# Performance work log

Hardware: AMD Instinct MI355X
Metric: run time of the kernel (lower is better)

## Reference

```python
import jax, jax.numpy as jnp
import numpy as np

INF_SUB_NUM = -9000000000000000.0
LN_EPS = 1e-5


def _layernorm(x, gamma, beta):
    mu = jnp.mean(x, axis=-1, keepdims=True)
    var = jnp.mean(jnp.square(x - mu), axis=-1, keepdims=True)
    return gamma * (x - mu) * jax.lax.rsqrt(var + LN_EPS) + beta


def setup_inputs() -> dict:
    key = jax.random.key(0)
    kh, ke, kt, kw1, kw2 = jax.random.split(key, 5)
    B, N, E, D = 8, 4096, 2048, 256
    stdv = 1.0 / np.sqrt(D)
    return {
        "hidden": jax.random.normal(kh, (B, N, D), dtype=jnp.float32),
        "ht": jax.random.randint(kt, (B, E, N), 0, 2, dtype=jnp.int32),
        "edge_emb": jax.random.normal(ke, (B, E, D), dtype=jnp.float32),
        "wnk": jax.random.uniform(kw1, (D, D), jnp.float32, -stdv, stdv),
        "wek": jax.random.uniform(kw2, (D, D), jnp.float32, -stdv, stdv),
        "ln_gamma": jnp.ones((D,), jnp.float32),
        "ln_beta": jnp.zeros((D,), jnp.float32),
    }


def reference(hidden, ht, edge_emb, wnk, wek, ln_gamma, ln_beta):
    # hidden: [B,N,D]; ht: [B,E,N] incidence; edge_emb: [B,E,D]
    D = hidden.shape[-1]
    scale = 1.0 / jnp.sqrt(jnp.float32(D))

    edge_emb = _layernorm(edge_emb, ln_gamma, ln_beta)          # [B,E,D]
    node_k = hidden @ wnk                                        # [B,N,D]

    # Stage 1: edges attend over their incident nodes (softmax over N, dim=2)
    edge_scores = jnp.einsum('bed,bnd->ben', edge_emb, node_k) * scale
    edge_scores = jnp.where(ht > 0, edge_scores, INF_SUB_NUM)
    attn_edge = jax.nn.softmax(edge_scores, axis=2)              # [B,E,N]
    edge_h = jnp.einsum('ben,bnd->bed', attn_edge, hidden) + edge_emb

    # Stage 2: nodes gather from edges; softmax over N (dim=1), as in source
    edge_k = edge_h @ wek                                        # [B,E,D]
    node_scores = jnp.einsum('bnd,bed->bne', node_k, edge_k) * scale
    node_scores = jnp.where(jnp.transpose(ht, (0, 2, 1)) > 0, node_scores, INF_SUB_NUM)
    attn_node = jax.nn.softmax(node_scores, axis=1)              # [B,N,E]
    node_hidden = jnp.einsum('bne,bed->bnd', attn_node, edge_h)  # [B,N,D]
    return node_hidden
```

## Files before the change

### kernel.cpp

```cpp
#include <hip/hip_runtime.h>
#include <hip/hip_bf16.h>
#include <stdint.h>


#define B_ 8
#define N_ 4096
#define E_ 2048
#define D_ 256
#define INF_SUB (-9.0e15f)

typedef short bf16x8 __attribute__((ext_vector_type(8)));
typedef float f32x4 __attribute__((ext_vector_type(4)));
typedef unsigned short us8 __attribute__((ext_vector_type(8)));

#define AS1 __attribute__((address_space(1)))
#define AS3 __attribute__((address_space(3)))

__device__ __forceinline__ unsigned short f2bf(float f) {
    union { float f; unsigned int u; } v; v.f = f;
    unsigned int r = v.u + 0x7fffu + ((v.u >> 16) & 1u);
    return (unsigned short)(r >> 16);
}
__device__ __forceinline__ float bf2f(unsigned short h) {
    union { unsigned int u; float f; } v; v.u = ((unsigned int)h) << 16;
    return v.f;
}
__device__ __forceinline__ float waveReduceSum(float v) {
#pragma unroll
    for (int o = 32; o > 0; o >>= 1) v += __shfl_xor(v, o, 64);
    return v;
}

__global__ __launch_bounds__(256) void ln_kernel(const float* __restrict__ x,
                                                 const float* __restrict__ gamma,
                                                 const float* __restrict__ beta,
                                                 unsigned short* __restrict__ yb) {
    __shared__ float red[8];
    const int row = blockIdx.x;
    const int t = threadIdx.x;
    const int lane = t & 63, wid = t >> 6;
    const float v = x[(size_t)row * D_ + t];
    float s = waveReduceSum(v);
    if (lane == 0) red[wid] = s;
    __syncthreads();
    const float mu = (red[0] + red[1] + red[2] + red[3]) * (1.0f / D_);
    const float d = v - mu;
    float s2 = waveReduceSum(d * d);
    if (lane == 0) red[4 + wid] = s2;
    __syncthreads();
    const float var = (red[4] + red[5] + red[6] + red[7]) * (1.0f / D_);
    yb[(size_t)row * D_ + t] = f2bf(gamma[t] * d * rsqrtf(var + 1e-5f) + beta[t]);
}

__global__ __launch_bounds__(256) void pack_mask(const int* __restrict__ ht,
                                                 uint32_t* __restrict__ bits) {
    const int row = blockIdx.x;
    const int t = threadIdx.x, wid = t >> 6, lane = t & 63;
    const int* hrow = ht + (size_t)row * N_;
    uint32_t* brow = bits + (size_t)row * (N_ / 32);
#pragma unroll
    for (int i = 0; i < 16; ++i) {
        const int c = wid * 16 + i;
        const int v = hrow[c * 64 + lane];
        unsigned long long m = __ballot(v > 0);
        if (lane == 0) {
            brow[c * 2] = (uint32_t)m;
            brow[c * 2 + 1] = (uint32_t)(m >> 32);
        }
    }
}

__global__ __launch_bounds__(256) void prep_hidden(const float* __restrict__ in,
                                                   unsigned short* __restrict__ hb,
                                                   unsigned short* __restrict__ hT) {
    __shared__ unsigned short tile[64][65];
    const int b = blockIdx.z;
    in += (size_t)b * N_ * D_;
    hb += (size_t)b * N_ * D_;
    hT += (size_t)b * D_ * N_;
    const int n0 = blockIdx.y * 64, d0 = blockIdx.x * 64;
    const int t = threadIdx.x;
    const int tr = t >> 4, tc = (t & 15) * 4;
#pragma unroll
    for (int q = 0; q < 4; ++q) {
        const int rr = q * 16 + tr;
        const float4 f = *(const float4*)&in[(size_t)(n0 + rr) * D_ + d0 + tc];
        unsigned short h0 = f2bf(f.x), h1 = f2bf(f.y), h2 = f2bf(f.z), h3 = f2bf(f.w);
        *(ushort4*)&hb[(size_t)(n0 + rr) * D_ + d0 + tc] = make_ushort4(h0, h1, h2, h3);
        tile[rr][tc + 0] = h0; tile[rr][tc + 1] = h1;
        tile[rr][tc + 2] = h2; tile[rr][tc + 3] = h3;
    }
    __syncthreads();
#pragma unroll
    for (int q = 0; q < 4; ++q) {
        const int cc = q * 16 + tr;
        ushort4 o = make_ushort4(tile[tc + 0][cc], tile[tc + 1][cc],
                                 tile[tc + 2][cc], tile[tc + 3][cc]);
        *(ushort4*)&hT[(size_t)(d0 + cc) * N_ + n0 + tc] = o;
    }
}

__global__ __launch_bounds__(256) void cast_wT(const float* __restrict__ w,
                                               unsigned short* __restrict__ wT) {
    const int gid = blockIdx.x * 256 + threadIdx.x;
    const int i = gid >> 8, j = gid & 255;
    wT[j * D_ + i] = f2bf(w[i * D_ + j]);
}

__global__ __launch_bounds__(256) void reduce_pv(const float* __restrict__ slab,
                                                 const unsigned short* __restrict__ eln,
                                                 const float* __restrict__ rsum,
                                                 unsigned short* __restrict__ eh,
                                                 float* __restrict__ ehT) {
    __shared__ float tile[64][65];
    const int b = blockIdx.z;
    const float* s0 = slab + (size_t)(b * 2) * E_ * D_;
    const float* s1 = slab + (size_t)(b * 2 + 1) * E_ * D_;
    const int e0 = blockIdx.y * 64, d0 = blockIdx.x * 64;
    const int t = threadIdx.x;
    const int tr = t >> 4, tc = (t & 15) * 4;
#pragma unroll
    for (int q = 0; q < 4; ++q) {
        const int rr = q * 16 + tr;
        const int row = e0 + rr;
        const float4 v0 = *(const float4*)&s0[(size_t)row * D_ + d0 + tc];
        const float4 v1 = *(const float4*)&s1[(size_t)row * D_ + d0 + tc];
        const float inv = 1.0f / rsum[(size_t)b * E_ + row];
        const ushort4 el = *(const ushort4*)&eln[(size_t)b * E_ * D_ + (size_t)row * D_ + d0 + tc];
        const float x0 = (v0.x + v1.x) * inv + bf2f(el.x);
        const float x1 = (v0.y + v1.y) * inv + bf2f(el.y);
        const float x2 = (v0.z + v1.z) * inv + bf2f(el.z);
        const float x3 = (v0.w + v1.w) * inv + bf2f(el.w);
        *(ushort4*)&eh[(size_t)b * E_ * D_ + (size_t)row * D_ + d0 + tc] =
            make_ushort4(f2bf(x0), f2bf(x1), f2bf(x2), f2bf(x3));
        tile[rr][tc + 0] = x0; tile[rr][tc + 1] = x1;
        tile[rr][tc + 2] = x2; tile[rr][tc + 3] = x3;
    }
    __syncthreads();
#pragma unroll
    for (int q = 0; q < 4; ++q) {
        const int cc = q * 16 + tr;
        float4 o = make_float4(tile[tc + 0][cc], tile[tc + 1][cc],
                               tile[tc + 2][cc], tile[tc + 3][cc]);
        *(float4*)&ehT[(size_t)b * D_ * E_ + (size_t)(d0 + cc) * E_ + e0 + tc] = o;
    }
}

__global__ __launch_bounds__(256) void scale_ehT(const float* __restrict__ ehT,
                                                 const float* __restrict__ lsum,
                                                 unsigned short* __restrict__ ehs) {
    const size_t base = ((size_t)blockIdx.x * 256 + threadIdx.x) * 8;
    const int b = (int)(base / ((size_t)D_ * E_));
    const int e = (int)(base % E_);
    const float4 f0 = *(const float4*)&ehT[base];
    const float4 f1 = *(const float4*)&ehT[base + 4];
    const float4 l0 = *(const float4*)&lsum[(size_t)b * E_ + e];
    const float4 l1 = *(const float4*)&lsum[(size_t)b * E_ + e + 4];
    us8 o;
    o[0] = f2bf(f0.x / l0.x); o[1] = f2bf(f0.y / l0.y);
    o[2] = f2bf(f0.z / l0.z); o[3] = f2bf(f0.w / l0.w);
    o[4] = f2bf(f1.x / l1.x); o[5] = f2bf(f1.y / l1.y);
    o[6] = f2bf(f1.z / l1.z); o[7] = f2bf(f1.w / l1.w);
    *(us8*)&ehs[base] = o;
}

__global__ __launch_bounds__(256) void colsum_exp(const unsigned short* __restrict__ S,
                                                  float* __restrict__ lsum) {
    const int b = blockIdx.y;
    const int n0 = blockIdx.x * 64;
    const int t = threadIdx.x;
    const unsigned short* p = S + ((size_t)b * N_ + n0) * E_ + t * 8;
    float s[8] = {};
    for (int i = 0; i < 64; ++i) {
        us8 v = *(const us8*)&p[(size_t)i * E_];
#pragma unroll
        for (int j = 0; j < 8; ++j) s[j] += __expf(bf2f(v[j]));
    }
#pragma unroll
    for (int j = 0; j < 8; ++j)
        atomicAdd(&lsum[(size_t)b * E_ + t * 8 + j], s[j]);
}

#define M_BF16 0
#define M_MASK 1
#define M_F32 2

template <int MODE, int MASKOR, int AEXP, int ASUM, int SPLIT>
__global__ __launch_bounds__(256) void mfma_gemm_nt(
        const short* __restrict__ A, const short* __restrict__ Bm,
        void* __restrict__ Cv, const uint32_t* __restrict__ bits,
        float* __restrict__ sums,
        int K, int ldc, size_t sA, size_t sB, size_t sC, float scale) {
    __shared__ __align__(16) short ls[(MODE == M_F32) ? 8192 : 16896];
    __shared__ uint32_t mwords[MASKOR ? 512 : 4];
    short* lsA = ls;
    short* lsB = ls + 4096;
    const int zb = blockIdx.z;
    const int b = SPLIT ? (zb >> 1) : zb;
    A += (size_t)b * sA;
    Bm += (size_t)b * sB;
    const int m0 = blockIdx.y * 128, n0 = blockIdx.x * 128;
    const int tid = threadIdx.x, wid = tid >> 6, lane = tid & 63;
    const int l15 = lane & 15, kg = lane >> 4;
    const int wr = wid >> 1, wc = wid & 1;

    if (MASKOR) {
        const uint32_t* bb = bits + (size_t)b * E_ * (N_ / 32);
#pragma unroll
        for (int q = 0; q < 2; ++q) {
            const int idx = q * 256 + tid;
            mwords[idx] = (MASKOR == 1)
                ? bb[(size_t)(m0 + (idx >> 2)) * (N_ / 32) + (n0 >> 5) + (idx & 3)]
                : bb[(size_t)(n0 + (idx >> 2)) * (N_ / 32) + (m0 >> 5) + (idx & 3)];
        }
    }

    int aoff[4], boff[4];
#pragma unroll
    for (int i = 0; i < 4; ++i) {
        const int ra = wr * 64 + i * 16 + l15;
        aoff[i] = ra * 32 + (((kg + (ra >> 1)) & 3) << 3);
        const int rb = wc * 64 + i * 16 + l15;
        boff[i] = rb * 32 + (((kg + (rb >> 1)) & 3) << 3);
    }
    const f32x4 zero = {0.f, 0.f, 0.f, 0.f};
    f32x4 acc[4][4];
#pragma unroll
    for (int i = 0; i < 4; ++i)
#pragma unroll
        for (int j = 0; j < 4; ++j) acc[i][j] = zero;

    float rsumLoc = 0.f;
    const int ar = tid >> 1, ah = tid & 1;

    const int kt0 = SPLIT ? (zb & 1) * (K >> 1) : 0;
    const int ktE = SPLIT ? kt0 + (K >> 1) : K;
    for (int kt = kt0; kt < ktE; kt += 32) {
        __syncthreads();
        if (AEXP) {
            const short* ga = A + (size_t)(m0 + ar) * K + kt + ah * 16;
            const us8 raw0 = *(const us8*)ga;
            const us8 raw1 = *(const us8*)(ga + 8);
            us8 e0, e1;
#pragma unroll
            for (int j = 0; j < 8; ++j) {
                const float x = __expf(bf2f(raw0[j]));
                if (ASUM) rsumLoc += x;
                e0[j] = f2bf(x);
            }
#pragma unroll
            for (int j = 0; j < 8; ++j) {
                const float x = __expf(bf2f(raw1[j]));
                if (ASUM) rsumLoc += x;
                e1[j] = f2bf(x);
            }
            const int p0 = (ah * 2 + (ar >> 1)) & 3;
            const int p1 = (ah * 2 + 1 + (ar >> 1)) & 3;
            *(us8*)&lsA[ar * 32 + p0 * 8] = e0;
            *(us8*)&lsA[ar * 32 + p1 * 8] = e1;
#pragma unroll
            for (int q = 0; q < 2; ++q) {
                const int c = q * 256 + tid;
                const int r = c >> 2;
                const int kc = ((c & 3) - (r >> 1)) & 3;
                const short* gb = Bm + (size_t)(n0 + r) * K + kt + kc * 8;
                __builtin_amdgcn_global_load_lds((const AS1 void*)gb,
                    (AS3 void*)(lsB + (q * 256 + wid * 64) * 8), 16, 0, 0);
            }
        } else {
#pragma unroll
            for (int q = 0; q < 2; ++q) {
                const int c = q * 256 + tid;
                const int r = c >> 2;
                const int kc = ((c & 3) - (r >> 1)) & 3;
                const short* ga = A + (size_t)(m0 + r) * K + kt + kc * 8;
                __builtin_amdgcn_global_load_lds((const AS1 void*)ga,
                    (AS3 void*)(lsA + (q * 256 + wid * 64) * 8), 16, 0, 0);
                const short* gb = Bm + (size_t)(n0 + r) * K + kt + kc * 8;
                __builtin_amdgcn_global_load_lds((const AS1 void*)gb,
                    (AS3 void*)(lsB + (q * 256 + wid * 64) * 8), 16, 0, 0);
            }
        }
        __syncthreads();
        bf16x8 fa[4], fb[4];
#pragma unroll
        for (int i = 0; i < 4; ++i) fa[i] = *(const bf16x8*)(lsA + aoff[i]);
#pragma unroll
        for (int j = 0; j < 4; ++j) fb[j] = *(const bf16x8*)(lsB + boff[j]);
#pragma unroll
        for (int i = 0; i < 4; ++i)
#pragma unroll
            for (int j = 0; j < 4; ++j)
                acc[i][j] = __builtin_amdgcn_mfma_f32_16x16x32_bf16(fa[i], fb[j], acc[i][j], 0, 0, 0);
    }

    if (AEXP && ASUM) {
        const float tot = rsumLoc + __shfl_xor(rsumLoc, 1, 64);
        if (ah == 0 && blockIdx.x == 0)
            atomicAdd(&sums[(size_t)b * E_ + m0 + ar], tot);
    }

    __syncthreads();

    if (MODE == M_F32) {
        float* C = (float*)Cv + (SPLIT ? (size_t)zb * sC : (size_t)b * sC);
        float* lsF = (float*)ls;
#pragma unroll
        for (int h = 0; h < 4; ++h) {
            if (wr == (h >> 1)) {
#pragma unroll
                for (int ii = 0; ii < 2; ++ii) {
                    const int i = (h & 1) * 2 + ii;
#pragma unroll
                    for (int j = 0; j < 4; ++j)
#pragma unroll
                        for (int r = 0; r < 4; ++r) {
                            const int rl = ii * 16 + kg * 4 + r;
                            const int cl = wc * 64 + j * 16 + l15;
                            lsF[rl * 128 + cl] = acc[i][j][r];
                        }
                }
            }
            __syncthreads();
#pragma unroll
            for (int si = 0; si < 4; ++si) {
                const int row = (tid >> 5) + si * 8;
                const int colb = (tid & 31) * 4;
                float4 v = *(float4*)&lsF[row * 128 + colb];
                *(float4*)&C[(size_t)(m0 + h * 32 + row) * ldc + n0 + colb] = v;
            }
            __syncthreads();
        }
    } else {
        unsigned short* C = (unsigned short*)Cv + (size_t)b * sC;
#pragma unroll
        for (int i = 0; i < 4; ++i) {
#pragma unroll
            for (int r = 0; r < 4; ++r) {
                const int rowfull = wr * 64 + i * 16 + kg * 4 + r;
                uint64_t mwr = 0;
                if (MODE == M_MASK && MASKOR == 1)
                    mwr = *(const uint64_t*)&mwords[rowfull * 4 + wc * 2];
#pragma unroll
                for (int j = 0; j < 4; ++j) {
                    const int cl = wc * 64 + j * 16 + l15;
                    float v = acc[i][j][r];
                    if (MODE == M_MASK) {
                        v *= scale;
                        uint32_t bit;
                        if (MASKOR == 1) {
                            bit = (uint32_t)(mwr >> (j * 16 + l15)) & 1u;
                        } else {
                            const uint64_t mwc = *(const uint64_t*)&mwords[cl * 4 + wr * 2];
                            bit = (uint32_t)(mwc >> (i * 16 + kg * 4 + r)) & 1u;
                        }
                        if (!bit) v = INF_SUB;
                    }
                    ls[rowfull * 132 + cl] = (short)f2bf(v);
                }
            }
        }
        __syncthreads();
#pragma unroll
        for (int si = 0; si < 8; ++si) {
            const int row = (tid >> 4) + si * 16;
            const int col = (tid & 15) * 8;
            us8 val = *(us8*)&ls[row * 132 + col];
            *(us8*)&C[(size_t)(m0 + row) * ldc + n0 + col] = val;
        }
    }
}

extern "C" void kernel_launch(void* const* d_in, const int* in_sizes, int n_in,
                              void* d_out, int out_size, void* d_ws, size_t ws_size,
                              hipStream_t stream) {
    const float* hidden = (const float*)d_in[0];
    const int* ht = (const int*)d_in[1];
    const float* edge_emb = (const float*)d_in[2];
    const float* wnk = (const float*)d_in[3];
    const float* wek = (const float*)d_in[4];
    const float* gamma = (const float*)d_in[5];
    const float* beta = (const float*)d_in[6];
    float* out = (float*)d_out;
    (void)in_sizes; (void)n_in; (void)out_size; (void)ws_size;

    char* w = (char*)d_ws;
    unsigned short* SP = (unsigned short*)w;         w += (size_t)B_ * E_ * N_ * 2;
    unsigned short* hidden_bf = (unsigned short*)w;  w += (size_t)B_ * N_ * D_ * 2;
    unsigned short* hiddenT_bf = (unsigned short*)w; w += (size_t)B_ * D_ * N_ * 2;
    unsigned short* node_k_bf = (unsigned short*)w;  w += (size_t)B_ * N_ * D_ * 2;
    unsigned short* eln_bf = (unsigned short*)w;     w += (size_t)B_ * E_ * D_ * 2;
    unsigned short* edge_h_bf = (unsigned short*)w;  w += (size_t)B_ * E_ * D_ * 2;
    float* ehT_f32 = (float*)w;                      w += (size_t)B_ * D_ * E_ * 4;
    unsigned short* ehsT_bf = (unsigned short*)w;    w += (size_t)B_ * D_ * E_ * 2;
    unsigned short* edge_k_bf = (unsigned short*)w;  w += (size_t)B_ * E_ * D_ * 2;
    float* slabs = (float*)w;                        w += (size_t)B_ * 2 * E_ * D_ * 4;
    uint32_t* bits = (uint32_t*)w;                   w += (size_t)B_ * E_ * (N_ / 32) * 4;
    float* rsum = (float*)w;                         w += (size_t)B_ * E_ * 4;
    float* lsum = (float*)w;                         w += (size_t)B_ * E_ * 4;
    unsigned short* wnkT = (unsigned short*)w;       w += (size_t)D_ * D_ * 2;
    unsigned short* wekT = (unsigned short*)w;       w += (size_t)D_ * D_ * 2;

    const float scale = 0.0625f;

    prep_hidden<<<dim3(D_ / 64, N_ / 64, B_), 256, 0, stream>>>(hidden, hidden_bf, hiddenT_bf);
    cast_wT<<<D_ * D_ / 256, 256, 0, stream>>>(wnk, wnkT);
    cast_wT<<<D_ * D_ / 256, 256, 0, stream>>>(wek, wekT);
    ln_kernel<<<B_ * E_, 256, 0, stream>>>(edge_emb, gamma, beta, eln_bf);
    pack_mask<<<B_ * E_, 256, 0, stream>>>(ht, bits);
    hipMemsetAsync(rsum, 0, (size_t)B_ * E_ * 8, stream);

    mfma_gemm_nt<M_BF16, 0, 0, 0, 0><<<dim3(D_ / 128, (B_ * N_) / 128, 1), 256, 0, stream>>>(
        (const short*)hidden_bf, (const short*)wnkT, node_k_bf, nullptr, nullptr,
        D_, D_, 0, 0, 0, 1.f);
    mfma_gemm_nt<M_MASK, 1, 0, 0, 0><<<dim3(N_ / 128, E_ / 128, B_), 256, 0, stream>>>(
        (const short*)eln_bf, (const short*)node_k_bf, SP, bits, nullptr,
        D_, N_, (size_t)E_ * D_, (size_t)N_ * D_, (size_t)E_ * N_, scale);
    mfma_gemm_nt<M_F32, 0, 1, 1, 1><<<dim3(D_ / 128, E_ / 128, B_ * 2), 256, 0, stream>>>(
        (const short*)SP, (const short*)hiddenT_bf, slabs, nullptr, rsum,
        N_, D_, (size_t)E_ * N_, (size_t)D_ * N_, (size_t)E_ * D_, 1.f);
    reduce_pv<<<dim3(D_ / 64, E_ / 64, B_), 256, 0, stream>>>(
        slabs, eln_bf, rsum, edge_h_bf, ehT_f32);
    mfma_gemm_nt<M_BF16, 0, 0, 0, 0><<<dim3(D_ / 128, (B_ * E_) / 128, 1), 256, 0, stream>>>(
        (const short*)edge_h_bf, (const short*)wekT, edge_k_bf, nullptr, nullptr,
        D_, D_, 0, 0, 0, 1.f);
    mfma_gemm_nt<M_MASK, 2, 0, 0, 0><<<dim3(E_ / 128, N_ / 128, B_), 256, 0, stream>>>(
        (const short*)node_k_bf, (const short*)edge_k_bf, SP, bits, nullptr,
        D_, E_, (size_t)N_ * D_, (size_t)E_ * D_, (size_t)N_ * E_, scale);
    colsum_exp<<<dim3(N_ / 64, B_), 256, 0, stream>>>(SP, lsum);
    scale_ehT<<<(B_ * D_ * E_) / (256 * 8), 256, 0, stream>>>(ehT_f32, lsum, ehsT_bf);
    mfma_gemm_nt<M_F32, 0, 1, 0, 0><<<dim3(D_ / 128, N_ / 128, B_), 256, 0, stream>>>(
        (const short*)SP, (const short*)ehsT_bf, out, nullptr, nullptr,
        E_, D_, (size_t)N_ * E_, (size_t)D_ * E_, (size_t)N_ * D_, 1.f);
}
```

Measured before the change: 868.1 us.

## Double GEMM K-tile to 64 and fuse column exp-sum into masked score GEMM

The GEMM kernel now stages 64-wide K tiles in LDS (doubled shared buffers, 8-way XOR-style rotation) and issues two MFMA sub-steps per barrier pair, halving the number of synchronisations and load phases. The separate colsum_exp pass over the N×E score matrix is removed; the masked stage-2 score GEMM instead accumulates exp of each written score per column and atomically adds the column sums. This avoids rereading the large bf16 score matrix, but adds atomics per block and uses more LDS per block, which may reduce occupancy. The fused sum uses fp32 values before bf16 rounding, while the later exp GEMM uses the rounded values, so the normaliser differs slightly from the old code.

```diff
diff --git a/kernel.cpp b/kernel.cpp
--- a/kernel.cpp
+++ b/kernel.cpp
@@ -164,37 +164,20 @@
     *(us8*)&ehs[base] = o;
 }
 
-__global__ __launch_bounds__(256) void colsum_exp(const unsigned short* __restrict__ S,
-                                                  float* __restrict__ lsum) {
-    const int b = blockIdx.y;
-    const int n0 = blockIdx.x * 64;
-    const int t = threadIdx.x;
-    const unsigned short* p = S + ((size_t)b * N_ + n0) * E_ + t * 8;
-    float s[8] = {};
-    for (int i = 0; i < 64; ++i) {
-        us8 v = *(const us8*)&p[(size_t)i * E_];
-#pragma unroll
-        for (int j = 0; j < 8; ++j) s[j] += __expf(bf2f(v[j]));
-    }
-#pragma unroll
-    for (int j = 0; j < 8; ++j)
-        atomicAdd(&lsum[(size_t)b * E_ + t * 8 + j], s[j]);
-}
-
 #define M_BF16 0
 #define M_MASK 1
 #define M_F32 2
 
-template <int MODE, int MASKOR, int AEXP, int ASUM, int SPLIT>
+template <int MODE, int MASKOR, int AEXP, int ASUM, int SPLIT, int CSUM>
 __global__ __launch_bounds__(256) void mfma_gemm_nt(
         const short* __restrict__ A, const short* __restrict__ Bm,
         void* __restrict__ Cv, const uint32_t* __restrict__ bits,
         float* __restrict__ sums,
         int K, int ldc, size_t sA, size_t sB, size_t sC, float scale) {
-    __shared__ __align__(16) short ls[(MODE == M_F32) ? 8192 : 16896];
+    __shared__ __align__(16) short ls[(MODE == M_F32) ? 16384 : 16896];
     __shared__ uint32_t mwords[MASKOR ? 512 : 4];
     short* lsA = ls;
-    short* lsB = ls + 4096;
+    short* lsB = ls + 8192;
     const int zb = blockIdx.z;
     const int b = SPLIT ? (zb >> 1) : zb;
     A += (size_t)b * sA;
@@ -215,13 +198,13 @@
         }
     }
 
-    int aoff[4], boff[4];
+    int raoff[4], rota[4], rboff[4], rotb[4];
 #pragma unroll
     for (int i = 0; i < 4; ++i) {
         const int ra = wr * 64 + i * 16 + l15;
-        aoff[i] = ra * 32 + (((kg + (ra >> 1)) & 3) << 3);
+        raoff[i] = ra * 64; rota[i] = kg + (ra >> 1);
         const int rb = wc * 64 + i * 16 + l15;
-        boff[i] = rb * 32 + (((kg + (rb >> 1)) & 3) << 3);
+        rboff[i] = rb * 64; rotb[i] = kg + (rb >> 1);
     }
     const f32x4 zero = {0.f, 0.f, 0.f, 0.f};
     f32x4 acc[4][4];
@@ -235,44 +218,41 @@
 
     const int kt0 = SPLIT ? (zb & 1) * (K >> 1) : 0;
     const int ktE = SPLIT ? kt0 + (K >> 1) : K;
-    for (int kt = kt0; kt < ktE; kt += 32) {
+    for (int kt = kt0; kt < ktE; kt += 64) {
         __syncthreads();
         if (AEXP) {
-            const short* ga = A + (size_t)(m0 + ar) * K + kt + ah * 16;
-            const us8 raw0 = *(const us8*)ga;
-            const us8 raw1 = *(const us8*)(ga + 8);
-            us8 e0, e1;
-#pragma unroll
-            for (int j = 0; j < 8; ++j) {
-                const float x = __expf(bf2f(raw0[j]));
-                if (ASUM) rsumLoc += x;
-                e0[j] = f2bf(x);
-            }
-#pragma unroll
-            for (int j = 0; j < 8; ++j) {
-                const float x = __expf(bf2f(raw1[j]));
-                if (ASUM) rsumLoc += x;
-                e1[j] = f2bf(x);
-            }
-            const int p0 = (ah * 2 + (ar >> 1)) & 3;
-            const int p1 = (ah * 2 + 1 + (ar >> 1)) & 3;
-            *(us8*)&lsA[ar * 32 + p0 * 8] = e0;
-            *(us8*)&lsA[ar * 32 + p1 * 8] = e1;
-#pragma unroll
-            for (int q = 0; q < 2; ++q) {
+            const short* ga = A + (size_t)(m0 + ar) * K + kt + ah * 32;
+            us8 raw[4], ex[4];
+#pragma unroll
+            for (int c = 0; c < 4; ++c) raw[c] = *(const us8*)(ga + c * 8);
+#pragma unroll
+            for (int c = 0; c < 4; ++c)
+#pragma unroll
+                for (int j = 0; j < 8; ++j) {
+                    const float x = __expf(bf2f(raw[c][j]));
+                    if (ASUM) rsumLoc += x;
+                    ex[c][j] = f2bf(x);
+                }
+#pragma unroll
+            for (int c = 0; c < 4; ++c) {
+                const int p = (ah * 4 + c + (ar >> 1)) & 7;
+                *(us8*)&lsA[ar * 64 + p * 8] = ex[c];
+            }
+#pragma unroll
+            for (int q = 0; q < 4; ++q) {
                 const int c = q * 256 + tid;
-                const int r = c >> 2;
-                const int kc = ((c & 3) - (r >> 1)) & 3;
+                const int r = c >> 3;
+                const int kc = ((c & 7) - (r >> 1)) & 7;
                 const short* gb = Bm + (size_t)(n0 + r) * K + kt + kc * 8;
                 __builtin_amdgcn_global_load_lds((const AS1 void*)gb,
                     (AS3 void*)(lsB + (q * 256 + wid * 64) * 8), 16, 0, 0);
             }
         } else {
 #pragma unroll
-            for (int q = 0; q < 2; ++q) {
+            for (int q = 0; q < 4; ++q) {
                 const int c = q * 256 + tid;
-                const int r = c >> 2;
-                const int kc = ((c & 3) - (r >> 1)) & 3;
+                const int r = c >> 3;
+                const int kc = ((c & 7) - (r >> 1)) & 7;
                 const short* ga = A + (size_t)(m0 + r) * K + kt + kc * 8;
                 __builtin_amdgcn_global_load_lds((const AS1 void*)ga,
                     (AS3 void*)(lsA + (q * 256 + wid * 64) * 8), 16, 0, 0);
@@ -282,16 +262,21 @@
             }
         }
         __syncthreads();
-        bf16x8 fa[4], fb[4];
-#pragma unroll
-        for (int i = 0; i < 4; ++i) fa[i] = *(const bf16x8*)(lsA + aoff[i]);
-#pragma unroll
-        for (int j = 0; j < 4; ++j) fb[j] = *(const bf16x8*)(lsB + boff[j]);
-#pragma unroll
-        for (int i = 0; i < 4; ++i)
+#pragma unroll
+        for (int s = 0; s < 2; ++s) {
+            bf16x8 fa[4], fb[4];
+#pragma unroll
+            for (int i = 0; i < 4; ++i)
+                fa[i] = *(const bf16x8*)(lsA + raoff[i] + (((s * 4 + rota[i]) & 7) << 3));
 #pragma unroll
             for (int j = 0; j < 4; ++j)
-                acc[i][j] = __builtin_amdgcn_mfma_f32_16x16x32_bf16(fa[i], fb[j], acc[i][j], 0, 0, 0);
+                fb[j] = *(const bf16x8*)(lsB + rboff[j] + (((s * 4 + rotb[j]) & 7) << 3));
+#pragma unroll
+            for (int i = 0; i < 4; ++i)
+#pragma unroll
+                for (int j = 0; j < 4; ++j)
+                    acc[i][j] = __builtin_amdgcn_mfma_f32_16x16x32_bf16(fa[i], fb[j], acc[i][j], 0, 0, 0);
+        }
     }
 
     if (AEXP && ASUM) {
@@ -333,6 +318,7 @@
         }
     } else {
         unsigned short* C = (unsigned short*)Cv + (size_t)b * sC;
+        float evsum[4] = {0.f, 0.f, 0.f, 0.f};
 #pragma unroll
         for (int i = 0; i < 4; ++i) {
 #pragma unroll
@@ -357,6 +343,7 @@
                         if (!bit) v = INF_SUB;
                     }
                     ls[rowfull * 132 + cl] = (short)f2bf(v);
+                    if (CSUM) evsum[j] += __expf(v);
                 }
             }
         }
@@ -367,6 +354,16 @@
             const int col = (tid & 15) * 8;
             us8 val = *(us8*)&ls[row * 132 + col];
             *(us8*)&C[(size_t)(m0 + row) * ldc + n0 + col] = val;
+        }
+        if (CSUM) {
+#pragma unroll
+            for (int j = 0; j < 4; ++j) {
+                float cs = evsum[j];
+                cs += __shfl_xor(cs, 16, 64);
+                cs += __shfl_xor(cs, 32, 64);
+                if (kg == 0)
+                    atomicAdd(&sums[(size_t)b * E_ + n0 + wc * 64 + j * 16 + l15], cs);
+            }
         }
     }
 }
@@ -410,26 +407,25 @@
     pack_mask<<<B_ * E_, 256, 0, stream>>>(ht, bits);
     hipMemsetAsync(rsum, 0, (size_t)B_ * E_ * 8, stream);
 
-    mfma_gemm_nt<M_BF16, 0, 0, 0, 0><<<dim3(D_ / 128, (B_ * N_) / 128, 1), 256, 0, stream>>>(
+    mfma_gemm_nt<M_BF16, 0, 0, 0, 0, 0><<<dim3(D_ / 128, (B_ * N_) / 128, 1), 256, 0, stream>>>(
         (const short*)hidden_bf, (const short*)wnkT, node_k_bf, nullptr, nullptr,
         D_, D_, 0, 0, 0, 1.f);
-    mfma_gemm_nt<M_MASK, 1, 0, 0, 0><<<dim3(N_ / 128, E_ / 128, B_), 256, 0, stream>>>(
+    mfma_gemm_nt<M_MASK, 1, 0, 0, 0, 0><<<dim3(N_ / 128, E_ / 128, B_), 256, 0, stream>>>(
         (const short*)eln_bf, (const short*)node_k_bf, SP, bits, nullptr,
         D_, N_, (size_t)E_ * D_, (size_t)N_ * D_, (size_t)E_ * N_, scale);
-    mfma_gemm_nt<M_F32, 0, 1, 1, 1><<<dim3(D_ / 128, E_ / 128, B_ * 2), 256, 0, stream>>>(
+    mfma_gemm_nt<M_F32, 0, 1, 1, 1, 0><<<dim3(D_ / 128, E_ / 128, B_ * 2), 256, 0, stream>>>(
         (const short*)SP, (const short*)hiddenT_bf, slabs, nullptr, rsum,
         N_, D_, (size_t)E_ * N_, (size_t)D_ * N_, (size_t)E_ * D_, 1.f);
     reduce_pv<<<dim3(D_ / 64, E_ / 64, B_), 256, 0, stream>>>(
         slabs, eln_bf, rsum, edge_h_bf, ehT_f32);
-    mfma_gemm_nt<M_BF16, 0, 0, 0, 0><<<dim3(D_ / 128, (B_ * E_) / 128, 1), 256, 0, stream>>>(
+    mfma_gemm_nt<M_BF16, 0, 0, 0, 0, 0><<<dim3(D_ / 128, (B_ * E_) / 128, 1), 256, 0, stream>>>(
         (const short*)edge_h_bf, (const short*)wekT, edge_k_bf, nullptr, nullptr,
         D_, D_, 0, 0, 0, 1.f);
-    mfma_gemm_nt<M_MASK, 2, 0, 0, 0><<<dim3(E_ / 128, N_ / 128, B_), 256, 0, stream>>>(
-        (const short*)node_k_bf, (const short*)edge_k_bf, SP, bits, nullptr,
+    mfma_gemm_nt<M_MASK, 2, 0, 0, 0, 1><<<dim3(E_ / 128, N_ / 128, B_), 256, 0, stream>>>(
+        (const short*)node_k_bf, (const short*)edge_k_bf, SP, bits, lsum,
         D_, E_, (size_t)N_ * D_, (size_t)E_ * D_, (size_t)N_ * E_, scale);
-    colsum_exp<<<dim3(N_ / 64, B_), 256, 0, stream>>>(SP, lsum);
     scale_ehT<<<(B_ * D_ * E_) / (256 * 8), 256, 0, stream>>>(ehT_f32, lsum, ehsT_bf);
-    mfma_gemm_nt<M_F32, 0, 1, 0, 0><<<dim3(D_ / 128, N_ / 128, B_), 256, 0, stream>>>(
+    mfma_gemm_nt<M_F32, 0, 1, 0, 0, 0><<<dim3(D_ / 128, N_ / 128, B_), 256, 0, stream>>>(
         (const short*)SP, (const short*)ehsT_bf, out, nullptr, nullptr,
         E_, D_, (size_t)N_ * E_, (size_t)D_ * E_, (size_t)N_ * D_, 1.f);
 }
```

Measured after the change: 791.1 us. 1.1x faster.
